# Performance work log

Measured on AMD Instinct MI355X. Metric: run time of the kernel, lower is better.

## Reference

```python
import jax, jax.numpy as jnp
import numpy as np

BS, N_NODES, T = 64, 1024, 1200


def _conv1d(h, w, b, stride, pad):
    # h: (N, 1, L), w: (1, 1, k) -> Conv1d(1,1,k,stride,pad) + bias
    y = jax.lax.conv_general_dilated(h, w, (stride,), [(pad, pad)],
                                     dimension_numbers=("NCH", "OIH", "NCH"))
    return y + b[None, :, None]


def _maxpool1d(h, k):
    # kernel=k, stride=k (PyTorch default stride=None -> kernel_size), VALID
    return jax.lax.reduce_window(h, -jnp.inf, jax.lax.max, (1, 1, k), (1, 1, k), "VALID")


def _gcn_ones_adj(h, W, b, n):
    # GCNConv with A = ones(n,n): A_hat = A + I, deg = n+1 uniformly,
    agg = (h + h.sum(axis=1, keepdims=True)) / (n + 1.0)
    return jnp.einsum("bnf,fg->bng", agg, W) + b


def setup_inputs() -> dict:
    key = jax.random.key(0)
    ks = jax.random.split(key, 16)
    p = lambda k, shp: jax.random.normal(k, shp, dtype=jnp.float32) * 0.1
    return {
        "x": jax.random.normal(ks[0], (BS, N_NODES, T), dtype=jnp.float32),
        "c0_w": p(ks[1], (1, 1, 2)), "c0_b": p(ks[2], (1,)),
        "c2_w": p(ks[3], (1, 1, 4)), "c2_b": p(ks[4], (1,)),
        "c4_w": p(ks[5], (1, 1, 4)), "c4_b": p(ks[6], (1,)),
        "c6_w": p(ks[7], (1, 1, 4)), "c6_b": p(ks[8], (1,)),
        "c8_w": p(ks[9], (1, 1, 3)), "c8_b": p(ks[10], (1,)),
        "gcn1_w": p(ks[11], (50, 50)), "gcn1_b": p(ks[12], (50,)),
        "gcn2_w": p(ks[13], (12, 12)), "gcn2_b": p(ks[14], (12,)),
        "cls_w": p(ks[15], (3, N_NODES)),
        "cls_b": jnp.zeros((3,), dtype=jnp.float32),
    }


def reference(x, c0_w, c0_b, c2_w, c2_b, c4_w, c4_b, c6_w, c6_b, c8_w, c8_b,
              gcn1_w, gcn1_b, gcn2_w, gcn2_b, cls_w, cls_b):
    bs, n, t = x.shape
    h = x.reshape(bs * n, 1, t)                 # batch all nodes together
    h = _conv1d(h, c0_w, c0_b, 2, 0)            # i=0: L=600
    h = jax.nn.relu(_maxpool1d(h, 3))           # i=1: L=200
    h = _conv1d(h, c2_w, c2_b, 2, 1)            # i=2: L=100
    h = jax.nn.relu(_maxpool1d(h, 2))           # i=3: L=50
    # i==4: source applies gcn1 to t_layer_out[4] AFTER it was consumed -> dead code
    _ = _gcn_ones_adj(h.reshape(bs, n, -1), gcn1_w, gcn1_b, n)
    h = _conv1d(h, c4_w, c4_b, 2, 1)            # i=4: L=25
    h = jax.nn.relu(_maxpool1d(h, 2))           # i=5: L=12
    # i==6: same dead-code pattern for gcn2
    _ = _gcn_ones_adj(h.reshape(bs, n, -1), gcn2_w, gcn2_b, n)
    h = _conv1d(h, c6_w, c6_b, 2, 1)            # i=6: L=6
    h = jax.nn.relu(_maxpool1d(h, 2))           # i=7: L=3
    h = _conv1d(h, c8_w, c8_b, 1, 0)            # i=8: L=1
    feat = h.reshape(bs, n)                     # (bs, n_nodes)
    logits = feat @ cls_w.T + cls_b
    return jax.nn.softmax(logits, axis=1)
```

## Files before the change

kernel.cpp:

```cpp
#include <hip/hip_runtime.h>
#include <math.h>

#define BS 64
#define NN 1024
#define T  1200
#define NSEQ (BS * NN)

#define WAVE_SYNC() asm volatile("s_waitcnt lgkmcnt(0)" ::: "memory")


__global__ __launch_bounds__(256) void chain_kernel(
    const float* __restrict__ x,
    const float* __restrict__ c0_w, const float* __restrict__ c0_b,
    const float* __restrict__ c2_w, const float* __restrict__ c2_b,
    const float* __restrict__ c4_w, const float* __restrict__ c4_b,
    const float* __restrict__ c6_w, const float* __restrict__ c6_b,
    const float* __restrict__ c8_w, const float* __restrict__ c8_b,
    float* __restrict__ feat)
{
    __shared__ __align__(16) float smem[4][1400];
    const int wave = threadIdx.x >> 6;
    const int lane = threadIdx.x & 63;
    const int seq  = blockIdx.x * 4 + wave;

    float* sx = smem[wave];
    float* sB = sx + 1200;

    const float w00 = c0_w[0], w01 = c0_w[1], b0 = c0_b[0];
    const float w20 = c2_w[0], w21 = c2_w[1], w22 = c2_w[2], w23 = c2_w[3], b2 = c2_b[0];
    const float w40 = c4_w[0], w41 = c4_w[1], w42 = c4_w[2], w43 = c4_w[3], b4 = c4_b[0];
    const float w60 = c6_w[0], w61 = c6_w[1], w62 = c6_w[2], w63 = c6_w[3], b6 = c6_b[0];
    const float w80 = c8_w[0], w81 = c8_w[1], w82 = c8_w[2], b8 = c8_b[0];

    const float4* xg4 = (const float4*)(x + (size_t)seq * T);
    float4* sx4 = (float4*)sx;
    float4 r0 = xg4[lane];
    float4 r1 = xg4[lane + 64];
    float4 r2 = xg4[lane + 128];
    float4 r3 = xg4[lane + 192];
    const bool tail = lane < 44;
    float4 r4 = make_float4(0.f, 0.f, 0.f, 0.f);
    if (tail) r4 = xg4[lane + 256];
    sx4[lane]       = r0;
    sx4[lane + 64]  = r1;
    sx4[lane + 128] = r2;
    sx4[lane + 192] = r3;
    if (tail) sx4[lane + 256] = r4;
    WAVE_SYNC();

#pragma unroll
    for (int it = 0; it < 4; ++it) {
        int p = lane + it * 64;
        if (p < 200) {
            const float* xp = sx + 6 * p;
            float x0 = xp[0], x1 = xp[1], x2 = xp[2], x3 = xp[3], x4 = xp[4], x5 = xp[5];
            float c0 = fmaf(w00, x0, fmaf(w01, x1, b0));
            float c1 = fmaf(w00, x2, fmaf(w01, x3, b0));
            float c2 = fmaf(w00, x4, fmaf(w01, x5, b0));
            sB[p] = fmaxf(fmaxf(fmaxf(c0, c1), c2), 0.0f);
        }
    }
    WAVE_SYNC();

    if (lane < 50) {
        int base = 4 * lane - 1;
        float v0 = sB[base < 0 ? 0 : base];
        float v1 = sB[base + 1];
        float v2 = sB[base + 2];
        float v3 = sB[base + 3];
        float v4 = sB[base + 4];
        float v5 = sB[(base + 5) > 199 ? 199 : (base + 5)];
        if (lane == 0)  v0 = 0.0f;
        if (lane == 49) v5 = 0.0f;
        float oa = fmaf(w20, v0, fmaf(w21, v1, fmaf(w22, v2, fmaf(w23, v3, b2))));
        float ob = fmaf(w20, v2, fmaf(w21, v3, fmaf(w22, v4, fmaf(w23, v5, b2))));
        sx[lane] = fmaxf(fmaxf(oa, ob), 0.0f);
    }
    WAVE_SYNC();

    if (lane < 12) {
        int base = 4 * lane - 1;
        float u0 = sx[base < 0 ? 0 : base];
        float u1 = sx[base + 1];
        float u2 = sx[base + 2];
        float u3 = sx[base + 3];
        float u4 = sx[base + 4];
        float u5 = sx[base + 5];
        if (lane == 0) u0 = 0.0f;
        float oa = fmaf(w40, u0, fmaf(w41, u1, fmaf(w42, u2, fmaf(w43, u3, b4))));
        float ob = fmaf(w40, u2, fmaf(w41, u3, fmaf(w42, u4, fmaf(w43, u5, b4))));
        sx[64 + lane] = fmaxf(fmaxf(oa, ob), 0.0f);
    }
    WAVE_SYNC();

    if (lane == 0) {
        float a3[14];
        a3[0] = 0.0f; a3[13] = 0.0f;
#pragma unroll
        for (int j = 0; j < 12; ++j) a3[j + 1] = sx[64 + j];
        float o[6];
#pragma unroll
        for (int j = 0; j < 6; ++j) {
            o[j] = fmaf(w60, a3[2 * j], fmaf(w61, a3[2 * j + 1],
                   fmaf(w62, a3[2 * j + 2], fmaf(w63, a3[2 * j + 3], b6))));
        }
        float A40 = fmaxf(fmaxf(o[0], o[1]), 0.0f);
        float A41 = fmaxf(fmaxf(o[2], o[3]), 0.0f);
        float A42 = fmaxf(fmaxf(o[4], o[5]), 0.0f);
        feat[seq] = fmaf(w80, A40, fmaf(w81, A41, fmaf(w82, A42, b8)));
    }
}

__global__ __launch_bounds__(256) void head_kernel(
    const float* __restrict__ feat,
    const float* __restrict__ cls_w,
    const float* __restrict__ cls_b,
    float* __restrict__ out)
{
    const int b = blockIdx.x;
    float a0 = 0.0f, a1 = 0.0f, a2 = 0.0f;
    for (int n = threadIdx.x; n < NN; n += 256) {
        float f = feat[b * NN + n];
        a0 += f * cls_w[0 * NN + n];
        a1 += f * cls_w[1 * NN + n];
        a2 += f * cls_w[2 * NN + n];
    }
    for (int off = 32; off; off >>= 1) {
        a0 += __shfl_down(a0, off);
        a1 += __shfl_down(a1, off);
        a2 += __shfl_down(a2, off);
    }
    __shared__ float red[4][3];
    const int wave = threadIdx.x >> 6;
    const int lane = threadIdx.x & 63;
    if (lane == 0) { red[wave][0] = a0; red[wave][1] = a1; red[wave][2] = a2; }
    __syncthreads();
    if (threadIdx.x == 0) {
        float l0 = red[0][0] + red[1][0] + red[2][0] + red[3][0] + cls_b[0];
        float l1 = red[0][1] + red[1][1] + red[2][1] + red[3][1] + cls_b[1];
        float l2 = red[0][2] + red[1][2] + red[2][2] + red[3][2] + cls_b[2];
        float m  = fmaxf(l0, fmaxf(l1, l2));
        float e0 = expf(l0 - m), e1 = expf(l1 - m), e2 = expf(l2 - m);
        float inv = 1.0f / (e0 + e1 + e2);
        out[b * 3 + 0] = e0 * inv;
        out[b * 3 + 1] = e1 * inv;
        out[b * 3 + 2] = e2 * inv;
    }
}

extern "C" void kernel_launch(void* const* d_in, const int* in_sizes, int n_in,
                              void* d_out, int out_size, void* d_ws, size_t ws_size,
                              hipStream_t stream) {
    const float* x     = (const float*)d_in[0];
    const float* c0_w  = (const float*)d_in[1];
    const float* c0_b  = (const float*)d_in[2];
    const float* c2_w  = (const float*)d_in[3];
    const float* c2_b  = (const float*)d_in[4];
    const float* c4_w  = (const float*)d_in[5];
    const float* c4_b  = (const float*)d_in[6];
    const float* c6_w  = (const float*)d_in[7];
    const float* c6_b  = (const float*)d_in[8];
    const float* c8_w  = (const float*)d_in[9];
    const float* c8_b  = (const float*)d_in[10];
    const float* cls_w = (const float*)d_in[15];
    const float* cls_b = (const float*)d_in[16];

    float* feat = (float*)d_ws;

    chain_kernel<<<NSEQ / 4, 256, 0, stream>>>(
        x, c0_w, c0_b, c2_w, c2_b, c4_w, c4_b, c6_w, c6_b, c8_w, c8_b, feat);
    head_kernel<<<BS, 256, 0, stream>>>(feat, cls_w, cls_b, (float*)d_out);
}
```

Measured before the change: 438.1 us.

## Make chain kernel persistent with register prefetch of next sequence

The chain kernel now launches a fixed 1024 blocks, and each wave loops over 16 sequences. It loads the next sequence's input into registers while computing the current one, overlapping global loads with shared-memory compute. This removes per-block launch overhead and hides load latency. In exchange it uses more registers, and the reduced grid may limit memory-level parallelism on a bandwidth-bound 315 MB read.

Measured after the change: 443.8 us, median of 2. Within noise of the previous version (+1.3%).

```diff
diff --git a/kernel.cpp b/kernel.cpp
--- a/kernel.cpp
+++ b/kernel.cpp
@@ -5,6 +5,10 @@
 #define NN 1024
 #define T  1200
 #define NSEQ (BS * NN)
+
+#define NBLK   1024
+#define WAVES  (NBLK * 4)
+#define ITERS  (NSEQ / WAVES)
 
 #define WAVE_SYNC() asm volatile("s_waitcnt lgkmcnt(0)" ::: "memory")
 
@@ -21,10 +25,11 @@
     __shared__ __align__(16) float smem[4][1400];
     const int wave = threadIdx.x >> 6;
     const int lane = threadIdx.x & 63;
-    const int seq  = blockIdx.x * 4 + wave;
+    const int wid  = blockIdx.x * 4 + wave;
 
     float* sx = smem[wave];
     float* sB = sx + 1200;
+    float4* sx4 = (float4*)sx;
 
     const float w00 = c0_w[0], w01 = c0_w[1], b0 = c0_b[0];
     const float w20 = c2_w[0], w21 = c2_w[1], w22 = c2_w[2], w23 = c2_w[3], b2 = c2_b[0];
@@ -32,82 +37,97 @@
     const float w60 = c6_w[0], w61 = c6_w[1], w62 = c6_w[2], w63 = c6_w[3], b6 = c6_b[0];
     const float w80 = c8_w[0], w81 = c8_w[1], w82 = c8_w[2], b8 = c8_b[0];
 
-    const float4* xg4 = (const float4*)(x + (size_t)seq * T);
-    float4* sx4 = (float4*)sx;
+    const bool tail = lane < 44;
+
+    const float4* xg4 = (const float4*)(x + (size_t)wid * T);
     float4 r0 = xg4[lane];
     float4 r1 = xg4[lane + 64];
     float4 r2 = xg4[lane + 128];
     float4 r3 = xg4[lane + 192];
-    const bool tail = lane < 44;
     float4 r4 = make_float4(0.f, 0.f, 0.f, 0.f);
     if (tail) r4 = xg4[lane + 256];
-    sx4[lane]       = r0;
-    sx4[lane + 64]  = r1;
-    sx4[lane + 128] = r2;
-    sx4[lane + 192] = r3;
-    if (tail) sx4[lane + 256] = r4;
-    WAVE_SYNC();
+
+    for (int it = 0; it < ITERS; ++it) {
+        const int seq = it * WAVES + wid;
+
+        sx4[lane]       = r0;
+        sx4[lane + 64]  = r1;
+        sx4[lane + 128] = r2;
+        sx4[lane + 192] = r3;
+        if (tail) sx4[lane + 256] = r4;
+        WAVE_SYNC();
+
+        if (it + 1 < ITERS) {
+            const float4* xn4 = (const float4*)(x + (size_t)(seq + WAVES) * T);
+            r0 = xn4[lane];
+            r1 = xn4[lane + 64];
+            r2 = xn4[lane + 128];
+            r3 = xn4[lane + 192];
+            if (tail) r4 = xn4[lane + 256];
+        }
 
 #pragma unroll
-    for (int it = 0; it < 4; ++it) {
-        int p = lane + it * 64;
-        if (p < 200) {
-            const float* xp = sx + 6 * p;
-            float x0 = xp[0], x1 = xp[1], x2 = xp[2], x3 = xp[3], x4 = xp[4], x5 = xp[5];
-            float c0 = fmaf(w00, x0, fmaf(w01, x1, b0));
-            float c1 = fmaf(w00, x2, fmaf(w01, x3, b0));
-            float c2 = fmaf(w00, x4, fmaf(w01, x5, b0));
-            sB[p] = fmaxf(fmaxf(fmaxf(c0, c1), c2), 0.0f);
+        for (int sub = 0; sub < 4; ++sub) {
+            int p = lane + sub * 64;
+            if (p < 200) {
+                const float* xp = sx + 6 * p;
+                float x0 = xp[0], x1 = xp[1], x2 = xp[2], x3 = xp[3], x4v = xp[4], x5 = xp[5];
+                float cA = fmaf(w00, x0, fmaf(w01, x1, b0));
+                float cB = fmaf(w00, x2, fmaf(w01, x3, b0));
+                float cC = fmaf(w00, x4v, fmaf(w01, x5, b0));
+                sB[p] = fmaxf(fmaxf(fmaxf(cA, cB), cC), 0.0f);
+            }
         }
-    }
-    WAVE_SYNC();
+        WAVE_SYNC();
 
-    if (lane < 50) {
-        int base = 4 * lane - 1;
-        float v0 = sB[base < 0 ? 0 : base];
-        float v1 = sB[base + 1];
-        float v2 = sB[base + 2];
-        float v3 = sB[base + 3];
-        float v4 = sB[base + 4];
-        float v5 = sB[(base + 5) > 199 ? 199 : (base + 5)];
-        if (lane == 0)  v0 = 0.0f;
-        if (lane == 49) v5 = 0.0f;
-        float oa = fmaf(w20, v0, fmaf(w21, v1, fmaf(w22, v2, fmaf(w23, v3, b2))));
-        float ob = fmaf(w20, v2, fmaf(w21, v3, fmaf(w22, v4, fmaf(w23, v5, b2))));
-        sx[lane] = fmaxf(fmaxf(oa, ob), 0.0f);
-    }
-    WAVE_SYNC();
+        if (lane < 50) {
+            int base = 4 * lane - 1;
+            float v0 = sB[base < 0 ? 0 : base];
+            float v1 = sB[base + 1];
+            float v2 = sB[base + 2];
+            float v3 = sB[base + 3];
+            float v4 = sB[base + 4];
+            float v5 = sB[(base + 5) > 199 ? 199 : (base + 5)];
+            if (lane == 0)  v0 = 0.0f;
+            if (lane == 49) v5 = 0.0f;
+            float oa = fmaf(w20, v0, fmaf(w21, v1, fmaf(w22, v2, fmaf(w23, v3, b2))));
+            float ob = fmaf(w20, v2, fmaf(w21, v3, fmaf(w22, v4, fmaf(w23, v5, b2))));
+            sx[lane] = fmaxf(fmaxf(oa, ob), 0.0f);
+        }
+        WAVE_SYNC();
 
-    if (lane < 12) {
-        int base = 4 * lane - 1;
-        float u0 = sx[base < 0 ? 0 : base];
-        float u1 = sx[base + 1];
-        float u2 = sx[base + 2];
-        float u3 = sx[base + 3];
-        float u4 = sx[base + 4];
-        float u5 = sx[base + 5];
-        if (lane == 0) u0 = 0.0f;
-        float oa = fmaf(w40, u0, fmaf(w41, u1, fmaf(w42, u2, fmaf(w43, u3, b4))));
-        float ob = fmaf(w40, u2, fmaf(w41, u3, fmaf(w42, u4, fmaf(w43, u5, b4))));
-        sx[64 + lane] = fmaxf(fmaxf(oa, ob), 0.0f);
-    }
-    WAVE_SYNC();
+        if (lane < 12) {
+            int base = 4 * lane - 1;
+            float u0 = sx[base < 0 ? 0 : base];
+            float u1 = sx[base + 1];
+            float u2 = sx[base + 2];
+            float u3 = sx[base + 3];
+            float u4 = sx[base + 4];
+            float u5 = sx[base + 5];
+            if (lane == 0) u0 = 0.0f;
+            float oa = fmaf(w40, u0, fmaf(w41, u1, fmaf(w42, u2, fmaf(w43, u3, b4))));
+            float ob = fmaf(w40, u2, fmaf(w41, u3, fmaf(w42, u4, fmaf(w43, u5, b4))));
+            sx[64 + lane] = fmaxf(fmaxf(oa, ob), 0.0f);
+        }
+        WAVE_SYNC();
 
-    if (lane == 0) {
-        float a3[14];
-        a3[0] = 0.0f; a3[13] = 0.0f;
+        if (lane == 0) {
+            float a3[14];
+            a3[0] = 0.0f; a3[13] = 0.0f;
 #pragma unroll
-        for (int j = 0; j < 12; ++j) a3[j + 1] = sx[64 + j];
-        float o[6];
+            for (int j = 0; j < 12; ++j) a3[j + 1] = sx[64 + j];
+            float o[6];
 #pragma unroll
-        for (int j = 0; j < 6; ++j) {
-            o[j] = fmaf(w60, a3[2 * j], fmaf(w61, a3[2 * j + 1],
-                   fmaf(w62, a3[2 * j + 2], fmaf(w63, a3[2 * j + 3], b6))));
+            for (int j = 0; j < 6; ++j) {
+                o[j] = fmaf(w60, a3[2 * j], fmaf(w61, a3[2 * j + 1],
+                       fmaf(w62, a3[2 * j + 2], fmaf(w63, a3[2 * j + 3], b6))));
+            }
+            float A40 = fmaxf(fmaxf(o[0], o[1]), 0.0f);
+            float A41 = fmaxf(fmaxf(o[2], o[3]), 0.0f);
+            float A42 = fmaxf(fmaxf(o[4], o[5]), 0.0f);
+            feat[seq] = fmaf(w80, A40, fmaf(w81, A41, fmaf(w82, A42, b8)));
         }
-        float A40 = fmaxf(fmaxf(o[0], o[1]), 0.0f);
-        float A41 = fmaxf(fmaxf(o[2], o[3]), 0.0f);
-        float A42 = fmaxf(fmaxf(o[4], o[5]), 0.0f);
-        feat[seq] = fmaf(w80, A40, fmaf(w81, A41, fmaf(w82, A42, b8)));
+        WAVE_SYNC();
     }
 }
 
@@ -167,7 +187,7 @@
 
     float* feat = (float*)d_ws;
 
-    chain_kernel<<<NSEQ / 4, 256, 0, stream>>>(
+    chain_kernel<<<NBLK, 256, 0, stream>>>(
         x, c0_w, c0_b, c2_w, c2_b, c4_w, c4_b, c6_w, c6_b, c8_w, c8_b, feat);
     head_kernel<<<BS, 256, 0, stream>>>(feat, cls_w, cls_b, (float*)d_out);
 }
```
